# Kernel optimization log

Measured on AMD Instinct MI355X. Metric: run time of the kernel, lower is better.

Reference implementation:

```python
import jax, jax.numpy as jnp
import numpy as np

B, T, D, H = 64, 512, 512, 1024


def setup_inputs() -> dict:
    key = jax.random.key(0)
    k0, k1, k2, k3, k4 = jax.random.split(key, 5)
    s0 = 1.0 / np.sqrt(D + H)   # torch nn.Linear init bound, layer 0
    s1 = 1.0 / np.sqrt(H + H)   # layer 1
    x = jax.random.normal(k0, (B, T, D), jnp.float32)
    W0 = jax.random.uniform(k1, (4 * H, D + H), jnp.float32, -s0, s0)
    b0 = jax.random.uniform(k2, (4 * H,), jnp.float32, -s0, s0)
    W1 = jax.random.uniform(k3, (4 * H, H + H), jnp.float32, -s1, s1)
    b1 = jax.random.uniform(k4, (4 * H,), jnp.float32, -s1, s1)
    return {"x": x, "W0": W0, "b0": b0, "W1": W1, "b1": b1}


def _lstm_layer(x, W, b):
    # x: (B, T, Din); W: (4H, Din+H); b: (4H,)
    hdim = b.shape[0] // 4
    bsz = x.shape[0]
    h0 = jnp.zeros((bsz, hdim), x.dtype)
    c0 = jnp.zeros((bsz, hdim), x.dtype)

    def step(carry, x_t):
        h, c = carry
        z = jnp.concatenate([x_t, h], axis=-1) @ W.T + b  # (B, 4H)
        i, f, o, g = jnp.split(z, 4, axis=-1)             # torch split order i,f,o,g
        c_next = jax.nn.sigmoid(f) * c + jax.nn.sigmoid(i) * jnp.tanh(g)
        h_next = jax.nn.sigmoid(o) * jnp.tanh(c_next)
        return (h_next, c_next), h_next

    (_, _), hs = jax.lax.scan(step, (h0, c0), jnp.swapaxes(x, 0, 1))
    return jnp.swapaxes(hs, 0, 1)  # (B, T, H)


def reference(x, W0, b0, W1, b1):
    y = _lstm_layer(x, W0, b0)
    y = _lstm_layer(y, W1, b1)
    return y  # last layer output sequence (return_all_layers=False)
```

## Files before the change

### kernel.cpp

```cpp
#include <hip/hip_runtime.h>
#include <hip/hip_bf16.h>

typedef __bf16 bf16x8 __attribute__((ext_vector_type(8)));
typedef float  f32x4  __attribute__((ext_vector_type(4)));

#define MFMA16(a, b, c) __builtin_amdgcn_mfma_f32_16x16x32_bf16((a), (b), (c), 0, 0, 0)

static constexpr int Bz = 64, Tz = 512, Dz = 512, Hz = 1024;
static constexpr int NWG0 = 128;
static constexpr int NWGT = 256;
static constexpr int NJ   = 8;

static constexpr size_t LDS_BYTES = 131072;

static constexpr size_t N_W0X = 4096ull * 512;
static constexpr size_t N_W0H = 4096ull * 1024;
static constexpr size_t N_W1  = 4096ull * 2048;
static constexpr size_t N_Y0  = 64ull * 512 * 1024;
static constexpr size_t N_X   = 64ull * 512 * 512;
static constexpr size_t OFF_W0XH = 0;
static constexpr size_t OFF_W0XL = OFF_W0XH + N_W0X;
static constexpr size_t OFF_W0H  = OFF_W0XL + N_W0X;
static constexpr size_t OFF_W1   = OFF_W0H  + N_W0H;
static constexpr size_t OFF_Y0   = OFF_W1   + N_W1;
static constexpr size_t FLAGS_BYTE = (((OFF_Y0 + N_Y0) * 2) + 255) & ~(size_t)255;
static constexpr size_t H1S_BYTE   = FLAGS_BYTE + 4096;
static constexpr size_t WS_NEED    = H1S_BYTE + N_Y0 * 2;
static constexpr size_t XHI_BYTE   = H1S_BYTE + N_Y0 * 2;
static constexpr size_t XLO_BYTE   = XHI_BYTE + N_X * 2;
static constexpr size_t WS_NEED_X  = XLO_BYTE + N_X * 2;

static constexpr int STEP_ELEMS = 65536;

__device__ __forceinline__ float sigm(float x) { return 1.0f / (1.0f + __expf(-x)); }

__device__ __forceinline__ void st_agent_u32(void* p, unsigned v)
{ __hip_atomic_store((unsigned*)p, v, __ATOMIC_RELAXED, __HIP_MEMORY_SCOPE_AGENT); }
__device__ __forceinline__ void st_agent_f32(float* p, float v)
{ __hip_atomic_store(p, v, __ATOMIC_RELAXED, __HIP_MEMORY_SCOPE_AGENT); }

extern "C" __global__ void prep_split(const float* __restrict__ x,
                                      const float* __restrict__ W0,
                                      const float* __restrict__ W1,
                                      __bf16* __restrict__ ws,
                                      __bf16* __restrict__ xhi,
                                      __bf16* __restrict__ xlo)
{
    if (blockIdx.x == 0)
        for (int i = threadIdx.x; i < 1024; i += 256)
            ((unsigned*)((char*)ws + FLAGS_BYTE))[i] = 0u;

    __bf16* w0xh = ws + OFF_W0XH;
    __bf16* w0xl = ws + OFF_W0XL;
    __bf16* w0h  = ws + OFF_W0H;
    __bf16* w1c  = ws + OFF_W1;
    const size_t ntot = N_W0X + N_W0H + N_W1;
    const size_t stride = (size_t)gridDim.x * blockDim.x;
    for (size_t idx = (size_t)blockIdx.x * blockDim.x + threadIdx.x;
         idx < ntot; idx += stride) {
        if (idx < N_W0X) {
            size_t r = idx >> 9, c = idx & 511;
            float w = W0[r * 1536 + c];
            __bf16 hi = (__bf16)w;
            w0xh[idx] = hi;
            w0xl[idx] = (__bf16)(w - (float)hi);
        } else if (idx < N_W0X + N_W0H) {
            size_t i = idx - N_W0X;
            size_t r = i >> 10, c = i & 1023;
            w0h[i] = (__bf16)W0[r * 1536 + 512 + c];
        } else {
            size_t i = idx - N_W0X - N_W0H;
            w1c[i] = (__bf16)W1[i];
        }
    }
    if (xhi) {
        for (size_t idx = (size_t)blockIdx.x * blockDim.x + threadIdx.x;
             idx < N_X; idx += stride) {
            float v = x[idx];
            __bf16 hi = (__bf16)v;
            xhi[idx] = hi;
            xlo[idx] = (__bf16)(v - (float)hi);
        }
    }
}

__device__ __forceinline__ void publish(unsigned* p, unsigned v)
{
    asm volatile("s_waitcnt vmcnt(0)" ::: "memory");
    __hip_atomic_store(p, v, __ATOMIC_RELAXED, __HIP_MEMORY_SCOPE_AGENT);
}

__device__ __forceinline__ void wait_chunk32(const unsigned* flags, int base, unsigned target)
{
    const unsigned* p = flags + base + (threadIdx.x & 31);
    for (;;) {
        unsigned v = __hip_atomic_load(p, __ATOMIC_RELAXED, __HIP_MEMORY_SCOPE_AGENT);
        if (__all(v >= target)) break;
        __builtin_amdgcn_s_sleep(1);
    }
    asm volatile("" ::: "memory");
}

__device__ __forceinline__ void zx_ps(const __bf16* __restrict__ xh,
                                      const __bf16* __restrict__ xl,
    const __bf16* wxh0, const __bf16* wxl0,
    const __bf16* wxh1, const __bf16* wxl1,
    f32x4& zx0, f32x4& zx1)
{
    f32x4 a0 = {0,0,0,0}, a1 = {0,0,0,0};
#pragma unroll 4
    for (int kk = 0; kk < Dz / 32; ++kk) {
        bf16x8 ahi = *(const bf16x8*)(xh + kk * 32);
        bf16x8 alo = *(const bf16x8*)(xl + kk * 32);
        bf16x8 wh0 = *(const bf16x8*)(wxh0 + kk * 1024);
        bf16x8 wl0 = *(const bf16x8*)(wxl0 + kk * 1024);
        bf16x8 wh1 = *(const bf16x8*)(wxh1 + kk * 1024);
        bf16x8 wl1 = *(const bf16x8*)(wxl1 + kk * 1024);
        a0 = MFMA16(ahi, wh0, a0); a0 = MFMA16(alo, wh0, a0); a0 = MFMA16(ahi, wl0, a0);
        a1 = MFMA16(ahi, wh1, a1); a1 = MFMA16(alo, wh1, a1); a1 = MFMA16(ahi, wl1, a1);
    }
    zx0 = a0; zx1 = a1;
}

__device__ __forceinline__ void zx_fb(const float* __restrict__ xt,
    const __bf16* wxh0, const __bf16* wxl0,
    const __bf16* wxh1, const __bf16* wxl1,
    f32x4& zx0, f32x4& zx1)
{
    f32x4 a0 = {0,0,0,0}, a1 = {0,0,0,0};
#pragma unroll 4
    for (int kk = 0; kk < Dz / 32; ++kk) {
        f32x4 va = *(const f32x4*)(xt + kk * 32);
        f32x4 vb = *(const f32x4*)(xt + kk * 32 + 4);
        bf16x8 ahi, alo;
#pragma unroll
        for (int e = 0; e < 4; ++e) {
            float v = va[e]; __bf16 h1 = (__bf16)v;
            ahi[e] = h1; alo[e] = (__bf16)(v - (float)h1);
            float w = vb[e]; __bf16 h2 = (__bf16)w;
            ahi[4 + e] = h2; alo[4 + e] = (__bf16)(w - (float)h2);
        }
        bf16x8 wh0 = *(const bf16x8*)(wxh0 + kk * 1024);
        bf16x8 wl0 = *(const bf16x8*)(wxl0 + kk * 1024);
        bf16x8 wh1 = *(const bf16x8*)(wxh1 + kk * 1024);
        bf16x8 wl1 = *(const bf16x8*)(wxl1 + kk * 1024);
        a0 = MFMA16(ahi, wh0, a0); a0 = MFMA16(alo, wh0, a0); a0 = MFMA16(ahi, wl0, a0);
        a1 = MFMA16(ahi, wh1, a1); a1 = MFMA16(alo, wh1, a1); a1 = MFMA16(ahi, wl1, a1);
    }
    zx0 = a0; zx1 = a1;
}

template <bool F32OUT>
__device__ __forceinline__ void gates_store(
    f32x4 za, f32x4 zb, float* cs, int lane, int l15, int rowBase,
    unsigned* yline, float* yf32, size_t rowStride)
{
    f32x4 pa, pb;
#pragma unroll
    for (int e = 0; e < 4; ++e) { pa[e] = __shfl_xor(za[e], 8, 64); pb[e] = __shfl_xor(zb[e], 8, 64); }
    const bool hi = (l15 & 8) != 0;
    int p01[2];
#pragma unroll
    for (int k2 = 0; k2 < 2; ++k2) {
        float zi, zf, zo, zg;
        if (hi) { zi = pa[2 + k2]; zf = za[2 + k2]; zo = pb[2 + k2]; zg = zb[2 + k2]; }
        else    { zi = za[k2];     zf = pa[k2];     zo = zb[k2];     zg = pb[k2];     }
        float cn = sigm(zf) * cs[k2] + sigm(zi) * tanhf(zg);
        float hn = sigm(zo) * tanhf(cn);
        cs[k2] = cn;
        if (F32OUT) {
            int b = rowBase + (hi ? 2 : 0) + k2;
            st_agent_f32(&yf32[(size_t)b * rowStride], hn);
        }
        __bf16 hb = (__bf16)hn;
        unsigned bits = (unsigned)__builtin_bit_cast(unsigned short, hb);
        unsigned par  = __shfl_down(bits, 1, 64);
        p01[k2] = (int)(bits | (par << 16));
    }
    if (yline) {
        int r    = lane >> 2;
        int srcl = ((r >> 2) << 4) | (((r >> 1) & 1) << 3) | ((lane & 3) << 1);
        unsigned v0 = (unsigned)__builtin_amdgcn_ds_bpermute(srcl * 4, p01[0]);
        unsigned v1 = (unsigned)__builtin_amdgcn_ds_bpermute(srcl * 4, p01[1]);
        st_agent_u32(yline + lane, (r & 1) ? v1 : v0);
    }
}

__device__ __forceinline__ void layer0(
    const float* __restrict__ x,
    const __bf16* __restrict__ xhi, const __bf16* __restrict__ xlo,
    const __bf16* __restrict__ w0xh, const __bf16* __restrict__ w0xl,
    const __bf16* __restrict__ w0h,  const float* __restrict__ b0,
    __bf16* y0, __bf16* wtile, unsigned* flags0)
{
    const int tid  = threadIdx.x;
    const int wave = tid >> 6, lane = tid & 63, l15 = lane & 15, lg = lane >> 4;
    const int wg   = blockIdx.x;
    const int j0   = wg * NJ;

    __bf16* sWXH = wtile;
    __bf16* sWXL = wtile + 16384;
    __bf16* sWH  = wtile + 32768;
    for (int idx = tid; idx < 32 * (Dz / 8); idx += 256) {
        int r = idx >> 6, k8 = idx & 63;
        int kk = k8 >> 2, sub = k8 & 3;
        int dst = kk * 1024 + r * 32 + ((sub * 8) ^ (((r >> 2) & 3) * 8));
        size_t grow = (size_t)((r >> 3) * Hz + j0 + (r & 7));
        *(bf16x8*)(sWXH + dst) = *(const bf16x8*)(w0xh + grow * Dz + k8 * 8);
        *(bf16x8*)(sWXL + dst) = *(const bf16x8*)(w0xl + grow * Dz + k8 * 8);
    }
    for (int idx = tid; idx < 32 * (Hz / 8); idx += 256) {
        int r = idx >> 7, k8 = idx & 127;
        int kk = k8 >> 2, sub = k8 & 3;
        int dst = kk * 1024 + r * 32 + ((sub * 8) ^ (((r >> 2) & 3) * 8));
        size_t grow = (size_t)((r >> 3) * Hz + j0 + (r & 7));
        *(bf16x8*)(sWH + dst) = *(const bf16x8*)(w0h + grow * Hz + k8 * 8);
    }
    __syncthreads();

    const __bf16* wxh[2]; const __bf16* wxl[2]; const __bf16* whp[2]; float bv[2];
#pragma unroll
    for (int tn = 0; tn < 2; ++tn) {
        int c = tn * 16 + l15;
        int lofs = c * 32 + ((lg * 8) ^ (((c >> 2) & 3) * 8));
        wxh[tn] = sWXH + lofs;
        wxl[tn] = sWXL + lofs;
        whp[tn] = sWH  + lofs;
        bv[tn]  = b0[(c >> 3) * Hz + j0 + (c & 7)];
    }
    const int bA = wave * 16 + l15;
    const float*  xp  = x + (size_t)bA * Tz * Dz + lg * 8;
    const __bf16* xph = xhi ? xhi + (size_t)bA * Tz * Dz + lg * 8 : nullptr;
    const __bf16* xpl = xlo ? xlo + (size_t)bA * Tz * Dz + lg * 8 : nullptr;
    const __bf16* hp0 = y0 + wave * 128 + l15 * 8 + lg * 512;

    const unsigned* flw = flags0 + wave * 128;
    unsigned* myflag     = flags0 + wave * 128 + wg;

    float cs[2] = {0.f, 0.f};
    f32x4 zx0, zx1;
    if (xph) zx_ps(xph, xpl, wxh[0], wxl[0], wxh[1], wxl[1], zx0, zx1);
    else     zx_fb(xp,       wxh[0], wxl[0], wxh[1], wxl[1], zx0, zx1);

    for (int s = 0; s < Tz; ++s) {
        f32x4 ah0 = {0,0,0,0}, ah1 = {0,0,0,0};
        if (s > 0) {
            const __bf16* ht = hp0 + (size_t)(s - 1) * STEP_ELEMS;
            for (int c4 = 0; c4 < 4; ++c4) {
                wait_chunk32(flw, 32 * c4, (unsigned)s);
#pragma unroll
                for (int kk = 8 * c4; kk < 8 * c4 + 8; ++kk) {
                    bf16x8 a = *(const bf16x8*)(ht + kk * 2048);
                    ah0 = MFMA16(a, *(const bf16x8*)(whp[0] + kk * 1024), ah0);
                    ah1 = MFMA16(a, *(const bf16x8*)(whp[1] + kk * 1024), ah1);
                }
            }
        }
        f32x4 za, zb;
#pragma unroll
        for (int e = 0; e < 4; ++e) { za[e] = zx0[e] + ah0[e] + bv[0]; zb[e] = zx1[e] + ah1[e] + bv[1]; }

        unsigned* yline = (unsigned*)y0 + (size_t)s * (STEP_ELEMS / 2) + wg * 256 + wave * 64;
        gates_store<false>(za, zb, cs, lane, l15, wave * 16 + lg * 4, yline, nullptr, 0);

        publish(myflag, (unsigned)(s + 1));
        if (s < Tz - 1) {
            if (xph) zx_ps(xph + (size_t)(s + 1) * Dz, xpl + (size_t)(s + 1) * Dz,
                           wxh[0], wxl[0], wxh[1], wxl[1], zx0, zx1);
            else     zx_fb(xp + (size_t)(s + 1) * Dz,
                           wxh[0], wxl[0], wxh[1], wxl[1], zx0, zx1);
        }
    }
}

__device__ __forceinline__ void layer1(
    const __bf16* __restrict__ y0, const __bf16* __restrict__ w1c,
    const float* __restrict__ b1, float* out, __bf16* h1s,
    __bf16* wtile, unsigned* flags0, unsigned* flags1)
{
    const int tid  = threadIdx.x;
    const int wave = tid >> 6, lane = tid & 63, l15 = lane & 15, lg = lane >> 4;
    const int wg   = blockIdx.x - NWG0;
    const int j0   = wg * NJ;

    __bf16* sWX = wtile;
    __bf16* sWH = wtile + 32768;
    for (int idx = tid; idx < 32 * (Hz / 8); idx += 256) {
        int r = idx >> 7, k8 = idx & 127;
        int kk = k8 >> 2, sub = k8 & 3;
        int dst = kk * 1024 + r * 32 + ((sub * 8) ^ (((r >> 2) & 3) * 8));
        size_t grow = (size_t)((r >> 3) * Hz + j0 + (r & 7));
        const __bf16* srow = w1c + grow * 2048;
        *(bf16x8*)(sWX + dst) = *(const bf16x8*)(srow + k8 * 8);
        *(bf16x8*)(sWH + dst) = *(const bf16x8*)(srow + 1024 + k8 * 8);
    }
    __syncthreads();

    const __bf16* wxp[2]; const __bf16* whp[2]; float bv[2];
#pragma unroll
    for (int tn = 0; tn < 2; ++tn) {
        int c = tn * 16 + l15;
        int lofs = c * 32 + ((lg * 8) ^ (((c >> 2) & 3) * 8));
        wxp[tn] = sWX + lofs;
        whp[tn] = sWH + lofs;
        bv[tn]  = b1[(c >> 3) * Hz + j0 + (c & 7)];
    }
    const int bA = wave * 16 + l15;
    const __bf16* xp0 = y0 + wave * 128 + l15 * 8 + lg * 512;
    const float*  hpf = out + (size_t)bA * Tz * Hz + lg * 8;
    const __bf16* hs0 = h1s ? h1s + wave * 128 + l15 * 8 + lg * 512 : nullptr;

    const unsigned* fl0w = flags0 + wave * 128;
    const unsigned* fl1w = flags1 + wave * 128;
    unsigned* myflag      = flags1 + wave * 128 + wg;

    float cs[2] = {0.f, 0.f};

    for (int s = 1; s <= Tz; ++s) {
        const int t = s - 1;
        f32x4 ax0 = {bv[0], bv[0], bv[0], bv[0]};
        f32x4 ax1 = {bv[1], bv[1], bv[1], bv[1]};

        if (t > 0) {
            if (hs0) {
                const __bf16* ht = hs0 + (size_t)(t - 1) * STEP_ELEMS;
                for (int c4 = 0; c4 < 4; ++c4) {
                    wait_chunk32(fl1w, 32 * c4, (unsigned)(s - 1));
#pragma unroll
                    for (int kk = 8 * c4; kk < 8 * c4 + 8; ++kk) {
                        bf16x8 a = *(const bf16x8*)(ht + kk * 2048);
                        ax0 = MFMA16(a, *(const bf16x8*)(whp[0] + kk * 1024), ax0);
                        ax1 = MFMA16(a, *(const bf16x8*)(whp[1] + kk * 1024), ax1);
                    }
                }
            } else {
                const float* ht = hpf + (size_t)(t - 1) * Hz;
                for (int c4 = 0; c4 < 4; ++c4) {
                    wait_chunk32(fl1w, 32 * c4, (unsigned)(s - 1));
#pragma unroll
                    for (int kk = 8 * c4; kk < 8 * c4 + 8; ++kk) {
                        f32x4 va = *(const f32x4*)(ht + kk * 32);
                        f32x4 vb = *(const f32x4*)(ht + kk * 32 + 4);
                        bf16x8 a;
#pragma unroll
                        for (int e = 0; e < 4; ++e) { a[e] = (__bf16)va[e]; a[4 + e] = (__bf16)vb[e]; }
                        ax0 = MFMA16(a, *(const bf16x8*)(whp[0] + kk * 1024), ax0);
                        ax1 = MFMA16(a, *(const bf16x8*)(whp[1] + kk * 1024), ax1);
                    }
                }
            }
        }
        {
            const __bf16* xt = xp0 + (size_t)t * STEP_ELEMS;
            for (int c4 = 0; c4 < 4; ++c4) {
                wait_chunk32(fl0w, 32 * c4, (unsigned)s);
#pragma unroll
                for (int kk = 8 * c4; kk < 8 * c4 + 8; ++kk) {
                    bf16x8 a = *(const bf16x8*)(xt + kk * 2048);
                    ax0 = MFMA16(a, *(const bf16x8*)(wxp[0] + kk * 1024), ax0);
                    ax1 = MFMA16(a, *(const bf16x8*)(wxp[1] + kk * 1024), ax1);
                }
            }
        }

        unsigned* hline = h1s ? (unsigned*)h1s + (size_t)t * (STEP_ELEMS / 2) + wg * 256 + wave * 64
                              : nullptr;
        gates_store<true>(ax0, ax1, cs, lane, l15, wave * 16 + lg * 4,
                          hline, out + (size_t)t * Hz + j0 + (l15 & 7), (size_t)Tz * Hz);

        if (s < Tz) publish(myflag, (unsigned)s);
    }
}

extern "C" __global__ void __launch_bounds__(256, 1)
lstm2(const float* __restrict__ x,
      const float* __restrict__ b0,
      const float* __restrict__ b1,
      __bf16* ws,
      float* out,
      __bf16* h1s,
      const __bf16* __restrict__ xhi,
      const __bf16* __restrict__ xlo)
{
    extern __shared__ char lds_raw[];
    __bf16* wtile = (__bf16*)lds_raw;
    unsigned* flags0 = (unsigned*)((char*)ws + FLAGS_BYTE);
    unsigned* flags1 = (unsigned*)((char*)ws + FLAGS_BYTE + 2048);

    if (blockIdx.x < NWG0)
        layer0(x, xhi, xlo, ws + OFF_W0XH, ws + OFF_W0XL, ws + OFF_W0H, b0,
               ws + OFF_Y0, wtile, flags0);
    else
        layer1(ws + OFF_Y0, ws + OFF_W1, b1, out, h1s, wtile, flags0, flags1);
}

extern "C" void kernel_launch(void* const* d_in, const int* in_sizes, int n_in,
                              void* d_out, int out_size, void* d_ws, size_t ws_size,
                              hipStream_t stream)
{
    const float* x  = (const float*)d_in[0];
    const float* W0 = (const float*)d_in[1];
    const float* b0 = (const float*)d_in[2];
    const float* W1 = (const float*)d_in[3];
    const float* b1 = (const float*)d_in[4];
    float* out = (float*)d_out;
    __bf16* ws = (__bf16*)d_ws;
    __bf16* h1s = (ws_size >= WS_NEED)   ? (__bf16*)((char*)ws + H1S_BYTE) : nullptr;
    __bf16* xhi = (ws_size >= WS_NEED_X) ? (__bf16*)((char*)ws + XHI_BYTE) : nullptr;
    __bf16* xlo = (ws_size >= WS_NEED_X) ? (__bf16*)((char*)ws + XLO_BYTE) : nullptr;

    (void)hipFuncSetAttribute((const void*)lstm2,
                        hipFuncAttributeMaxDynamicSharedMemorySize, (int)LDS_BYTES);

    hipLaunchKernelGGL(prep_split, dim3(2048), dim3(256), 0, stream, x, W0, W1, ws, xhi, xlo);

    const __bf16* xhic = xhi; const __bf16* xloc = xlo;
    void* args[] = { (void*)&x, (void*)&b0, (void*)&b1, (void*)&ws, (void*)&out,
                     (void*)&h1s, (void*)&xhic, (void*)&xloc };
    (void)hipLaunchCooperativeKernel(reinterpret_cast<void*>(lstm2),
                               dim3(NWGT), dim3(256), args, LDS_BYTES, stream);
}
```

Baseline: 5.212 ms.

## Co-locate both LSTM layers per workgroup and stream input weights from swizzled global images

Merges the separate layer-0 and layer-1 workgroups into 128 workgroups of 512 threads, where waves 0-3 run layer 0 and waves 4-7 run layer 1 for the same hidden slice. Only the recurrent weight tiles of both layers now sit in LDS. The input-projection weights are read from new pre-swizzled global images built in the prep kernel, and the precomputed split copies of x are dropped. The goal is to halve the number of workgroups taking part in flag synchronisation and to keep both layers on one CU. The cost is input weights read from global/L2 every step, half as many CUs doing work, and on-the-fly splitting of x.

```diff
diff --git a/kernel.cpp b/kernel.cpp
--- a/kernel.cpp
+++ b/kernel.cpp
@@ -7,9 +7,7 @@
 #define MFMA16(a, b, c) __builtin_amdgcn_mfma_f32_16x16x32_bf16((a), (b), (c), 0, 0, 0)
 
 static constexpr int Bz = 64, Tz = 512, Dz = 512, Hz = 1024;
-static constexpr int NWG0 = 128;
-static constexpr int NWGT = 256;
-static constexpr int NJ   = 8;
+static constexpr int NWG = 128;
 
 static constexpr size_t LDS_BYTES = 131072;
 
@@ -17,7 +15,6 @@
 static constexpr size_t N_W0H = 4096ull * 1024;
 static constexpr size_t N_W1  = 4096ull * 2048;
 static constexpr size_t N_Y0  = 64ull * 512 * 1024;
-static constexpr size_t N_X   = 64ull * 512 * 512;
 static constexpr size_t OFF_W0XH = 0;
 static constexpr size_t OFF_W0XL = OFF_W0XH + N_W0X;
 static constexpr size_t OFF_W0H  = OFF_W0XL + N_W0X;
@@ -26,9 +23,13 @@
 static constexpr size_t FLAGS_BYTE = (((OFF_Y0 + N_Y0) * 2) + 255) & ~(size_t)255;
 static constexpr size_t H1S_BYTE   = FLAGS_BYTE + 4096;
 static constexpr size_t WS_NEED    = H1S_BYTE + N_Y0 * 2;
-static constexpr size_t XHI_BYTE   = H1S_BYTE + N_Y0 * 2;
-static constexpr size_t XLO_BYTE   = XHI_BYTE + N_X * 2;
-static constexpr size_t WS_NEED_X  = XLO_BYTE + N_X * 2;
+static constexpr size_t IMG_BYTE   = H1S_BYTE + N_Y0 * 2;
+static constexpr size_t N_IMG0     = 128ull * 16384;
+static constexpr size_t N_IMG1     = 128ull * 32768;
+static constexpr size_t IMG0H_OFF  = 0;
+static constexpr size_t IMG0L_OFF  = IMG0H_OFF + N_IMG0;
+static constexpr size_t IMG1_OFF   = IMG0L_OFF + N_IMG0;
+static constexpr size_t WS_NEED_IMG = IMG_BYTE + (IMG1_OFF + N_IMG1) * 2;
 
 static constexpr int STEP_ELEMS = 65536;
 
@@ -43,8 +44,9 @@
                                       const float* __restrict__ W0,
                                       const float* __restrict__ W1,
                                       __bf16* __restrict__ ws,
-                                      __bf16* __restrict__ xhi,
-                                      __bf16* __restrict__ xlo)
+                                      __bf16* __restrict__ img0h,
+                                      __bf16* __restrict__ img0l,
+                                      __bf16* __restrict__ img1)
 {
     if (blockIdx.x == 0)
         for (int i = threadIdx.x; i < 1024; i += 256)
@@ -73,13 +75,31 @@
             w1c[i] = (__bf16)W1[i];
         }
     }
-    if (xhi) {
-        for (size_t idx = (size_t)blockIdx.x * blockDim.x + threadIdx.x;
-             idx < N_X; idx += stride) {
-            float v = x[idx];
-            __bf16 hi = (__bf16)v;
-            xhi[idx] = hi;
-            xlo[idx] = (__bf16)(v - (float)hi);
+    if (img0h) {
+        for (size_t g = (size_t)blockIdx.x * blockDim.x + threadIdx.x;
+             g < 262144; g += stride) {
+            int wg = (int)(g >> 11), c = (g >> 6) & 31, kk = (g >> 2) & 15, sub = g & 3;
+            size_t grow = (size_t)((c >> 3) * 1024 + wg * 8 + (c & 7));
+            const float* src = W0 + grow * 1536 + (kk * 4 + sub) * 8;
+            size_t dst = (size_t)wg * 16384 + kk * 1024 + c * 32
+                       + ((sub * 8) ^ (((c >> 2) & 3) * 8));
+#pragma unroll
+            for (int e = 0; e < 8; ++e) {
+                float v = src[e];
+                __bf16 hi = (__bf16)v;
+                img0h[dst + e] = hi;
+                img0l[dst + e] = (__bf16)(v - (float)hi);
+            }
+        }
+        for (size_t g = (size_t)blockIdx.x * blockDim.x + threadIdx.x;
+             g < 524288; g += stride) {
+            int wg = (int)(g >> 12), c = (g >> 7) & 31, kk = (g >> 2) & 31, sub = g & 3;
+            size_t grow = (size_t)((c >> 3) * 1024 + wg * 8 + (c & 7));
+            const float* src = W1 + grow * 2048 + (kk * 4 + sub) * 8;
+            size_t dst = (size_t)wg * 32768 + kk * 1024 + c * 32
+                       + ((sub * 8) ^ (((c >> 2) & 3) * 8));
+#pragma unroll
+            for (int e = 0; e < 8; ++e) img1[dst + e] = (__bf16)src[e];
         }
     }
 }
@@ -101,30 +121,9 @@
     asm volatile("" ::: "memory");
 }
 
-__device__ __forceinline__ void zx_ps(const __bf16* __restrict__ xh,
-                                      const __bf16* __restrict__ xl,
-    const __bf16* wxh0, const __bf16* wxl0,
-    const __bf16* wxh1, const __bf16* wxl1,
-    f32x4& zx0, f32x4& zx1)
-{
-    f32x4 a0 = {0,0,0,0}, a1 = {0,0,0,0};
-#pragma unroll 4
-    for (int kk = 0; kk < Dz / 32; ++kk) {
-        bf16x8 ahi = *(const bf16x8*)(xh + kk * 32);
-        bf16x8 alo = *(const bf16x8*)(xl + kk * 32);
-        bf16x8 wh0 = *(const bf16x8*)(wxh0 + kk * 1024);
-        bf16x8 wl0 = *(const bf16x8*)(wxl0 + kk * 1024);
-        bf16x8 wh1 = *(const bf16x8*)(wxh1 + kk * 1024);
-        bf16x8 wl1 = *(const bf16x8*)(wxl1 + kk * 1024);
-        a0 = MFMA16(ahi, wh0, a0); a0 = MFMA16(alo, wh0, a0); a0 = MFMA16(ahi, wl0, a0);
-        a1 = MFMA16(ahi, wh1, a1); a1 = MFMA16(alo, wh1, a1); a1 = MFMA16(ahi, wl1, a1);
-    }
-    zx0 = a0; zx1 = a1;
-}
-
 __device__ __forceinline__ void zx_fb(const float* __restrict__ xt,
     const __bf16* wxh0, const __bf16* wxl0,
-    const __bf16* wxh1, const __bf16* wxl1,
+    const __bf16* wxh1, const __bf16* wxl1, int wstr,
     f32x4& zx0, f32x4& zx1)
 {
     f32x4 a0 = {0,0,0,0}, a1 = {0,0,0,0};
@@ -140,10 +139,10 @@
             float w = vb[e]; __bf16 h2 = (__bf16)w;
             ahi[4 + e] = h2; alo[4 + e] = (__bf16)(w - (float)h2);
         }
-        bf16x8 wh0 = *(const bf16x8*)(wxh0 + kk * 1024);
-        bf16x8 wl0 = *(const bf16x8*)(wxl0 + kk * 1024);
-        bf16x8 wh1 = *(const bf16x8*)(wxh1 + kk * 1024);
-        bf16x8 wl1 = *(const bf16x8*)(wxl1 + kk * 1024);
+        bf16x8 wh0 = *(const bf16x8*)(wxh0 + kk * wstr);
+        bf16x8 wl0 = *(const bf16x8*)(wxl0 + kk * wstr);
+        bf16x8 wh1 = *(const bf16x8*)(wxh1 + kk * wstr);
+        bf16x8 wl1 = *(const bf16x8*)(wxl1 + kk * wstr);
         a0 = MFMA16(ahi, wh0, a0); a0 = MFMA16(alo, wh0, a0); a0 = MFMA16(ahi, wl0, a0);
         a1 = MFMA16(ahi, wh1, a1); a1 = MFMA16(alo, wh1, a1); a1 = MFMA16(ahi, wl1, a1);
     }
@@ -186,61 +185,39 @@
     }
 }
 
-__device__ __forceinline__ void layer0(
+__device__ __forceinline__ void layer0_wave(
+    int m, int lane, int l15, int lg, int wg, int j0,
     const float* __restrict__ x,
-    const __bf16* __restrict__ xhi, const __bf16* __restrict__ xlo,
-    const __bf16* __restrict__ w0xh, const __bf16* __restrict__ w0xl,
-    const __bf16* __restrict__ w0h,  const float* __restrict__ b0,
-    __bf16* y0, __bf16* wtile, unsigned* flags0)
-{
-    const int tid  = threadIdx.x;
-    const int wave = tid >> 6, lane = tid & 63, l15 = lane & 15, lg = lane >> 4;
-    const int wg   = blockIdx.x;
-    const int j0   = wg * NJ;
-
-    __bf16* sWXH = wtile;
-    __bf16* sWXL = wtile + 16384;
-    __bf16* sWH  = wtile + 32768;
-    for (int idx = tid; idx < 32 * (Dz / 8); idx += 256) {
-        int r = idx >> 6, k8 = idx & 63;
-        int kk = k8 >> 2, sub = k8 & 3;
-        int dst = kk * 1024 + r * 32 + ((sub * 8) ^ (((r >> 2) & 3) * 8));
-        size_t grow = (size_t)((r >> 3) * Hz + j0 + (r & 7));
-        *(bf16x8*)(sWXH + dst) = *(const bf16x8*)(w0xh + grow * Dz + k8 * 8);
-        *(bf16x8*)(sWXL + dst) = *(const bf16x8*)(w0xl + grow * Dz + k8 * 8);
-    }
-    for (int idx = tid; idx < 32 * (Hz / 8); idx += 256) {
-        int r = idx >> 7, k8 = idx & 127;
-        int kk = k8 >> 2, sub = k8 & 3;
-        int dst = kk * 1024 + r * 32 + ((sub * 8) ^ (((r >> 2) & 3) * 8));
-        size_t grow = (size_t)((r >> 3) * Hz + j0 + (r & 7));
-        *(bf16x8*)(sWH + dst) = *(const bf16x8*)(w0h + grow * Hz + k8 * 8);
-    }
-    __syncthreads();
-
+    const __bf16* sWh0,
+    const __bf16* __restrict__ ix_h, const __bf16* __restrict__ ix_l, int xstr,
+    const float* __restrict__ b0,
+    __bf16* y0, unsigned* flags0)
+{
     const __bf16* wxh[2]; const __bf16* wxl[2]; const __bf16* whp[2]; float bv[2];
 #pragma unroll
     for (int tn = 0; tn < 2; ++tn) {
         int c = tn * 16 + l15;
         int lofs = c * 32 + ((lg * 8) ^ (((c >> 2) & 3) * 8));
-        wxh[tn] = sWXH + lofs;
-        wxl[tn] = sWXL + lofs;
-        whp[tn] = sWH  + lofs;
-        bv[tn]  = b0[(c >> 3) * Hz + j0 + (c & 7)];
-    }
-    const int bA = wave * 16 + l15;
-    const float*  xp  = x + (size_t)bA * Tz * Dz + lg * 8;
-    const __bf16* xph = xhi ? xhi + (size_t)bA * Tz * Dz + lg * 8 : nullptr;
-    const __bf16* xpl = xlo ? xlo + (size_t)bA * Tz * Dz + lg * 8 : nullptr;
-    const __bf16* hp0 = y0 + wave * 128 + l15 * 8 + lg * 512;
-
-    const unsigned* flw = flags0 + wave * 128;
-    unsigned* myflag     = flags0 + wave * 128 + wg;
+        whp[tn] = sWh0 + lofs;
+        if (xstr == 1024) {
+            wxh[tn] = ix_h + (size_t)wg * 16384 + lofs;
+            wxl[tn] = ix_l + (size_t)wg * 16384 + lofs;
+        } else {
+            size_t grow = (size_t)((c >> 3) * 1024 + j0 + (c & 7));
+            wxh[tn] = ix_h + grow * Dz + lg * 8;
+            wxl[tn] = ix_l + grow * Dz + lg * 8;
+        }
+        bv[tn] = b0[(c >> 3) * Hz + j0 + (c & 7)];
+    }
+    const float*  xp  = x  + (size_t)(m * 16 + l15) * Tz * Dz + lg * 8;
+    const __bf16* hp0 = y0 + m * 128 + l15 * 8 + lg * 512;
+
+    const unsigned* flw = flags0 + m * 128;
+    unsigned* myflag     = flags0 + m * 128 + wg;
 
     float cs[2] = {0.f, 0.f};
     f32x4 zx0, zx1;
-    if (xph) zx_ps(xph, xpl, wxh[0], wxl[0], wxh[1], wxl[1], zx0, zx1);
-    else     zx_fb(xp,       wxh[0], wxl[0], wxh[1], wxl[1], zx0, zx1);
+    zx_fb(xp, wxh[0], wxl[0], wxh[1], wxl[1], xstr, zx0, zx1);
 
     for (int s = 0; s < Tz; ++s) {
         f32x4 ah0 = {0,0,0,0}, ah1 = {0,0,0,0};
@@ -260,59 +237,44 @@
 #pragma unroll
         for (int e = 0; e < 4; ++e) { za[e] = zx0[e] + ah0[e] + bv[0]; zb[e] = zx1[e] + ah1[e] + bv[1]; }
 
-        unsigned* yline = (unsigned*)y0 + (size_t)s * (STEP_ELEMS / 2) + wg * 256 + wave * 64;
-        gates_store<false>(za, zb, cs, lane, l15, wave * 16 + lg * 4, yline, nullptr, 0);
+        unsigned* yline = (unsigned*)y0 + (size_t)s * (STEP_ELEMS / 2) + wg * 256 + m * 64;
+        gates_store<false>(za, zb, cs, lane, l15, m * 16 + lg * 4, yline, nullptr, 0);
 
         publish(myflag, (unsigned)(s + 1));
-        if (s < Tz - 1) {
-            if (xph) zx_ps(xph + (size_t)(s + 1) * Dz, xpl + (size_t)(s + 1) * Dz,
-                           wxh[0], wxl[0], wxh[1], wxl[1], zx0, zx1);
-            else     zx_fb(xp + (size_t)(s + 1) * Dz,
-                           wxh[0], wxl[0], wxh[1], wxl[1], zx0, zx1);
-        }
-    }
-}
-
-__device__ __forceinline__ void layer1(
-    const __bf16* __restrict__ y0, const __bf16* __restrict__ w1c,
-    const float* __restrict__ b1, float* out, __bf16* h1s,
-    __bf16* wtile, unsigned* flags0, unsigned* flags1)
-{
-    const int tid  = threadIdx.x;
-    const int wave = tid >> 6, lane = tid & 63, l15 = lane & 15, lg = lane >> 4;
-    const int wg   = blockIdx.x - NWG0;
-    const int j0   = wg * NJ;
-
-    __bf16* sWX = wtile;
-    __bf16* sWH = wtile + 32768;
-    for (int idx = tid; idx < 32 * (Hz / 8); idx += 256) {
-        int r = idx >> 7, k8 = idx & 127;
-        int kk = k8 >> 2, sub = k8 & 3;
-        int dst = kk * 1024 + r * 32 + ((sub * 8) ^ (((r >> 2) & 3) * 8));
-        size_t grow = (size_t)((r >> 3) * Hz + j0 + (r & 7));
-        const __bf16* srow = w1c + grow * 2048;
-        *(bf16x8*)(sWX + dst) = *(const bf16x8*)(srow + k8 * 8);
-        *(bf16x8*)(sWH + dst) = *(const bf16x8*)(srow + 1024 + k8 * 8);
-    }
-    __syncthreads();
-
+        if (s < Tz - 1)
+            zx_fb(xp + (size_t)(s + 1) * Dz, wxh[0], wxl[0], wxh[1], wxl[1], xstr, zx0, zx1);
+    }
+}
+
+__device__ __forceinline__ void layer1_wave(
+    int m, int lane, int l15, int lg, int wg, int j0,
+    const __bf16* __restrict__ y0,
+    const __bf16* sWh1,
+    const __bf16* __restrict__ ix1, int xstr,
+    const float* __restrict__ b1,
+    float* out, __bf16* h1s, unsigned* flags0, unsigned* flags1)
+{
     const __bf16* wxp[2]; const __bf16* whp[2]; float bv[2];
 #pragma unroll
     for (int tn = 0; tn < 2; ++tn) {
         int c = tn * 16 + l15;
         int lofs = c * 32 + ((lg * 8) ^ (((c >> 2) & 3) * 8));
-        wxp[tn] = sWX + lofs;
-        whp[tn] = sWH + lofs;
-        bv[tn]  = b1[(c >> 3) * Hz + j0 + (c & 7)];
-    }
-    const int bA = wave * 16 + l15;
-    const __bf16* xp0 = y0 + wave * 128 + l15 * 8 + lg * 512;
-    const float*  hpf = out + (size_t)bA * Tz * Hz + lg * 8;
-    const __bf16* hs0 = h1s ? h1s + wave * 128 + l15 * 8 + lg * 512 : nullptr;
-
-    const unsigned* fl0w = flags0 + wave * 128;
-    const unsigned* fl1w = flags1 + wave * 128;
-    unsigned* myflag      = flags1 + wave * 128 + wg;
+        whp[tn] = sWh1 + lofs;
+        if (xstr == 1024) {
+            wxp[tn] = ix1 + (size_t)wg * 32768 + lofs;
+        } else {
+            size_t grow = (size_t)((c >> 3) * 1024 + j0 + (c & 7));
+            wxp[tn] = ix1 + grow * 2048 + lg * 8;
+        }
+        bv[tn] = b1[(c >> 3) * Hz + j0 + (c & 7)];
+    }
+    const __bf16* xp0 = y0 + m * 128 + l15 * 8 + lg * 512;
+    const float*  hpf = out + (size_t)(m * 16 + l15) * Tz * Hz + lg * 8;
+    const __bf16* hs0 = h1s ? h1s + m * 128 + l15 * 8 + lg * 512 : nullptr;
+
+    const unsigned* fl0w = flags0 + m * 128;
+    const unsigned* fl1w = flags1 + m * 128;
+    unsigned* myflag      = flags1 + m * 128 + wg;
 
     float cs[2] = {0.f, 0.f};
 
@@ -357,41 +319,68 @@
 #pragma unroll
                 for (int kk = 8 * c4; kk < 8 * c4 + 8; ++kk) {
                     bf16x8 a = *(const bf16x8*)(xt + kk * 2048);
-                    ax0 = MFMA16(a, *(const bf16x8*)(wxp[0] + kk * 1024), ax0);
-                    ax1 = MFMA16(a, *(const bf16x8*)(wxp[1] + kk * 1024), ax1);
+                    ax0 = MFMA16(a, *(const bf16x8*)(wxp[0] + kk * (xstr == 1024 ? 1024 : 32)), ax0);
+                    ax1 = MFMA16(a, *(const bf16x8*)(wxp[1] + kk * (xstr == 1024 ? 1024 : 32)), ax1);
                 }
             }
         }
 
-        unsigned* hline = h1s ? (unsigned*)h1s + (size_t)t * (STEP_ELEMS / 2) + wg * 256 + wave * 64
+        unsigned* hline = h1s ? (unsigned*)h1s + (size_t)t * (STEP_ELEMS / 2) + wg * 256 + m * 64
                               : nullptr;
-        gates_store<true>(ax0, ax1, cs, lane, l15, wave * 16 + lg * 4,
+        gates_store<true>(ax0, ax1, cs, lane, l15, m * 16 + lg * 4,
                           hline, out + (size_t)t * Hz + j0 + (l15 & 7), (size_t)Tz * Hz);
 
         if (s < Tz) publish(myflag, (unsigned)s);
     }
 }
 
-extern "C" __global__ void __launch_bounds__(256, 1)
+extern "C" __global__ void __launch_bounds__(512, 1)
 lstm2(const float* __restrict__ x,
       const float* __restrict__ b0,
       const float* __restrict__ b1,
       __bf16* ws,
       float* out,
       __bf16* h1s,
-      const __bf16* __restrict__ xhi,
-      const __bf16* __restrict__ xlo)
+      const __bf16* __restrict__ img0h,
+      const __bf16* __restrict__ img0l,
+      const __bf16* __restrict__ img1)
 {
     extern __shared__ char lds_raw[];
-    __bf16* wtile = (__bf16*)lds_raw;
+    __bf16* sWh0 = (__bf16*)lds_raw;
+    __bf16* sWh1 = (__bf16*)(lds_raw + 65536);
     unsigned* flags0 = (unsigned*)((char*)ws + FLAGS_BYTE);
     unsigned* flags1 = (unsigned*)((char*)ws + FLAGS_BYTE + 2048);
 
-    if (blockIdx.x < NWG0)
-        layer0(x, xhi, xlo, ws + OFF_W0XH, ws + OFF_W0XL, ws + OFF_W0H, b0,
-               ws + OFF_Y0, wtile, flags0);
-    else
-        layer1(ws + OFF_Y0, ws + OFF_W1, b1, out, h1s, wtile, flags0, flags1);
+    const int tid  = threadIdx.x;
+    const int wave = tid >> 6, lane = tid & 63, l15 = lane & 15, lg = lane >> 4;
+    const int wg   = blockIdx.x;
+    const int j0   = wg * 8;
+
+    const __bf16* w0h = ws + OFF_W0H;
+    const __bf16* w1c = ws + OFF_W1;
+    __bf16* y0        = ws + OFF_Y0;
+
+    for (int idx = tid; idx < 4096; idx += 512) {
+        int r = idx >> 7, k8 = idx & 127;
+        int kk = k8 >> 2, sub = k8 & 3;
+        int dst = kk * 1024 + r * 32 + ((sub * 8) ^ (((r >> 2) & 3) * 8));
+        size_t grow = (size_t)((r >> 3) * Hz + j0 + (r & 7));
+        *(bf16x8*)(sWh0 + dst) = *(const bf16x8*)(w0h + grow * Hz + k8 * 8);
+        *(bf16x8*)(sWh1 + dst) = *(const bf16x8*)(w1c + grow * 2048 + 1024 + k8 * 8);
+    }
+    __syncthreads();
+
+    const bool haveImg = (img0h != nullptr);
+    if (wave < 4) {
+        const __bf16* ih = haveImg ? img0h : ws + OFF_W0XH;
+        const __bf16* il = haveImg ? img0l : ws + OFF_W0XL;
+        layer0_wave(wave, lane, l15, lg, wg, j0, x, sWh0,
+                    ih, il, haveImg ? 1024 : 32, b0, y0, flags0);
+    } else {
+        const __bf16* i1 = haveImg ? img1 : w1c;
+        layer1_wave(wave - 4, lane, l15, lg, wg, j0, y0, sWh1,
+                    i1, haveImg ? 1024 : 32, b1, out, h1s, flags0, flags1);
+    }
 }
 
 extern "C" void kernel_launch(void* const* d_in, const int* in_sizes, int n_in,
@@ -405,18 +394,22 @@
     const float* b1 = (const float*)d_in[4];
     float* out = (float*)d_out;
     __bf16* ws = (__bf16*)d_ws;
-    __bf16* h1s = (ws_size >= WS_NEED)   ? (__bf16*)((char*)ws + H1S_BYTE) : nullptr;
-    __bf16* xhi = (ws_size >= WS_NEED_X) ? (__bf16*)((char*)ws + XHI_BYTE) : nullptr;
-    __bf16* xlo = (ws_size >= WS_NEED_X) ? (__bf16*)((char*)ws + XLO_BYTE) : nullptr;
+    __bf16* h1s = (ws_size >= WS_NEED) ? (__bf16*)((char*)ws + H1S_BYTE) : nullptr;
+
+    __bf16* imgBase = (ws_size >= WS_NEED_IMG) ? (__bf16*)((char*)ws + IMG_BYTE) : nullptr;
+    __bf16* img0h = imgBase ? imgBase + IMG0H_OFF : nullptr;
+    __bf16* img0l = imgBase ? imgBase + IMG0L_OFF : nullptr;
+    __bf16* img1  = imgBase ? imgBase + IMG1_OFF  : nullptr;
 
     (void)hipFuncSetAttribute((const void*)lstm2,
                         hipFuncAttributeMaxDynamicSharedMemorySize, (int)LDS_BYTES);
 
-    hipLaunchKernelGGL(prep_split, dim3(2048), dim3(256), 0, stream, x, W0, W1, ws, xhi, xlo);
-
-    const __bf16* xhic = xhi; const __bf16* xloc = xlo;
+    hipLaunchKernelGGL(prep_split, dim3(2048), dim3(256), 0, stream,
+                       x, W0, W1, ws, img0h, img0l, img1);
+
+    const __bf16* i0h = img0h; const __bf16* i0l = img0l; const __bf16* i1 = img1;
     void* args[] = { (void*)&x, (void*)&b0, (void*)&b1, (void*)&ws, (void*)&out,
-                     (void*)&h1s, (void*)&xhic, (void*)&xloc };
+                     (void*)&h1s, (void*)&i0h, (void*)&i0l, (void*)&i1 };
     (void)hipLaunchCooperativeKernel(reinterpret_cast<void*>(lstm2),
-                               dim3(NWGT), dim3(256), args, LDS_BYTES, stream);
-}
+                               dim3(NWG), dim3(512), args, LDS_BYTES, stream);
+}
```

New measurement: 14.14 ms. 2.71x slower.
